# Performance work log

Hardware: AMD Instinct MI355X
Metric: run time of the kernel (lower is better)

The kernel has to match this reference:

```python
import jax, jax.numpy as jnp
import numpy as np

B, T, C, H = 16, 2048, 192, 64

def setup_inputs() -> dict:
    key = jax.random.key(0)
    k1, k2, k3, k4 = jax.random.split(key, 4)
    x = jax.random.normal(k1, (B, T, C), dtype=jnp.float32)
    Wq = jax.random.normal(k2, (C, H), dtype=jnp.float32) * (C ** -0.5)
    Wk = jax.random.normal(k3, (C, H), dtype=jnp.float32) * (C ** -0.5)
    Wv = jax.random.normal(k4, (C, H), dtype=jnp.float32) * (C ** -0.5)
    return {"x": x, "Wq": Wq, "Wk": Wk, "Wv": Wv}

def reference(x, Wq, Wk, Wv):
    # One head of causal self-attention (dropout in eval mode / identity).
    q = x @ Wq                       # [B, T, H]
    k = x @ Wk                       # [B, T, H]
    v = x @ Wv                       # [B, T, H]
    scale = q.shape[-1] ** -0.5
    wei = jnp.einsum('bth,bsh->bts', q, k) * scale   # [B, T, T]
    t = wei.shape[-1]
    causal = jnp.tril(jnp.ones((t, t), dtype=bool))  # tril mask
    wei = jnp.where(causal, wei, -jnp.inf)
    wei = jax.nn.softmax(wei, axis=-1)
    out = jnp.einsum('bts,bsh->bth', wei, v)         # [B, T, H]
    return out
```

## Files before the change

### kernel.cpp

```cpp
#include <hip/hip_runtime.h>

#define B 16
#define T 2048
#define C 192
#define H 64

typedef __bf16 bf16x8 __attribute__((ext_vector_type(8)));
typedef __bf16 bf16x4 __attribute__((ext_vector_type(4)));
typedef float  f32x4  __attribute__((ext_vector_type(4)));

#define MFMA(a, b, c) __builtin_amdgcn_mfma_f32_16x16x32_bf16(a, b, c, 0, 0, 0)

#define SM_BIAS 24.0f

__global__ __launch_bounds__(512) void wtrans_kernel(
    const float* __restrict__ Wq, const float* __restrict__ Wk,
    const float* __restrict__ Wv, __bf16* __restrict__ Wf)
{
    const int idx  = blockIdx.x * 512 + threadIdx.x;
    const int ntg  = idx / 384;
    const int rem  = idx - ntg * 384;
    const int kc   = rem >> 6;
    const int lane = rem & 63;
    const float* Wm = (ntg < 4) ? Wq : (ntg < 8) ? Wk : Wv;
    const int nl = ((ntg & 3) << 4) + (lane & 15);
    const int k0 = kc * 32 + (lane >> 4) * 8;
    bf16x8 d;
    #pragma unroll
    for (int j = 0; j < 8; j++) d[j] = (__bf16)Wm[(k0 + j) * H + nl];
    *(bf16x8*)(Wf + (size_t)idx * 8) = d;
}

__global__ __launch_bounds__(512, 4) void qkv_mfma_kernel(
    const float* __restrict__ x,
    const __bf16* __restrict__ Wf,
    __bf16* __restrict__ qb, __bf16* __restrict__ kb, __bf16* __restrict__ vt)
{
    __shared__ __bf16 tile[64][72];

    const int tid  = threadIdx.x;
    const int w    = tid >> 6;
    const int wg   = w >> 2;
    const int wr   = w & 3;
    const int lane = tid & 63;
    const int lid  = tid & 15;
    const int quad = lane >> 4;
    const int m0   = blockIdx.x * 64 + wr * 16;

    const float* xrow = x + (size_t)(m0 + lid) * C + quad * 8;
    bf16x8 af[6];
    #pragma unroll
    for (int kc = 0; kc < 6; kc++) {
        const float4 a0 = *(const float4*)(xrow + kc * 32);
        const float4 a1 = *(const float4*)(xrow + kc * 32 + 4);
        af[kc][0] = (__bf16)a0.x; af[kc][1] = (__bf16)a0.y;
        af[kc][2] = (__bf16)a0.z; af[kc][3] = (__bf16)a0.w;
        af[kc][4] = (__bf16)a1.x; af[kc][5] = (__bf16)a1.y;
        af[kc][6] = (__bf16)a1.z; af[kc][7] = (__bf16)a1.w;
    }

    f32x4 acc[6] = {};
    #pragma unroll
    for (int kc = 0; kc < 6; kc++)
        #pragma unroll
        for (int nt = 0; nt < 6; nt++) {
            const int ntg = wg * 6 + nt;
            const bf16x8 bfr = *(const bf16x8*)(
                Wf + (((size_t)(ntg * 6 + kc)) * 64 + lane) * 8);
            acc[nt] = MFMA(af[kc], bfr, acc[nt]);
        }

    #pragma unroll
    for (int nt = 0; nt < 6; nt++) {
        const int ntg = wg * 6 + nt;
        const int n = ntg * 16 + lid;
        if (ntg < 8) {
            __bf16* dst = (ntg < 4) ? qb : kb;
            const int col = n & 63;
            const float scale = (ntg < 4) ? 0.1803368801111204f : 1.0f;
            #pragma unroll
            for (int r = 0; r < 4; r++) {
                const int row = m0 + quad * 4 + r;
                dst[(size_t)row * H + col] = (__bf16)(acc[nt][r] * scale);
            }
        } else {
            const int col = n - 128;
            #pragma unroll
            for (int r = 0; r < 4; r++)
                tile[wr * 16 + quad * 4 + r][col] = (__bf16)(acc[nt][r]);
        }
    }
    __syncthreads();

    const int bb = blockIdx.x >> 5;
    const int t0 = (blockIdx.x & 31) << 6;
    {
        const int h   = tid >> 3;
        const int tl0 = (tid & 7) * 8;
        bf16x8 d;
        #pragma unroll
        for (int j = 0; j < 8; j++) d[j] = tile[tl0 + j][h];
        *(bf16x8*)(vt + ((size_t)(bb * H + h)) * T + t0 + tl0) = d;
    }
}

__global__ __launch_bounds__(512, 4) void attn_kernel(
    const __bf16* __restrict__ qb,
    const __bf16* __restrict__ kb,
    const __bf16* __restrict__ vt,
    float* __restrict__ out)
{
    __shared__ __bf16 Kb[2][2][64][72];
    __shared__ __bf16 Vb[2][2][64][68];

    const int tid  = threadIdx.x;
    const int wv   = tid >> 6;
    const int grp  = wv >> 2;
    const int w    = wv & 3;
    const int lid  = tid & 15;
    const int quad = (tid & 63) >> 4;

    const int half = blockIdx.x >> 8;
    const int rem  = blockIdx.x & 255;
    const int b    = rem & 15;
    const int pr   = rem >> 4;
    const int qt   = half ? pr : (31 - pr);
    const int nch  = qt + 1;
    const int nsteps = (nch + 1) >> 1;
    const size_t bbase = (size_t)b * T;

    const int qX = (qt << 6) + w * 16;

    const __bf16* qr = qb + (bbase + qX + lid) * H + quad * 8;
    const bf16x8 qf0 = *(const bf16x8*)(qr);
    const bf16x8 qf1 = *(const bf16x8*)(qr + 32);

    const __bf16* kgb = kb + bbase * H;
    const __bf16* vgb = vt + (size_t)b * H * T;

    const int ra = tid >> 3, ca = (tid & 7) * 8;

    auto keyof = [&](int i) {
        if (i > nch - 1) i = nch - 1;
        return i << 6;
    };

    bf16x8 kr[2], vr2[2];
    auto prefetch = [&](int s) {
        #pragma unroll
        for (int g = 0; g < 2; g++) {
            const int key0 = keyof(2 * s + g);
            kr[g]  = *(const bf16x8*)(kgb + (size_t)(key0 + ra) * H + ca);
            vr2[g] = *(const bf16x8*)(vgb + (size_t)ra * T + key0 + ca);
        }
    };

    f32x4 O[4] = {};
    float ls = 0.f;

    auto doChunk = [&](int key0, int cur) {
        const __bf16 (*Kc)[72] = Kb[cur][grp];
        const __bf16 (*Vc)[68] = Vb[cur][grp];
        bf16x8 kf[8];
        #pragma unroll
        for (int j = 0; j < 4; j++) {
            kf[2*j]   = *(const bf16x8*)&Kc[j * 16 + lid][quad * 8];
            kf[2*j+1] = *(const bf16x8*)&Kc[j * 16 + lid][32 + quad * 8];
        }
        bf16x8 bv0[4], bv1[4];
        #pragma unroll
        for (int ht = 0; ht < 4; ht++) {
            const __bf16* vr_ = &Vc[ht * 16 + lid][quad * 4];
            ((bf16x4*)&bv0[ht])[0] = *(const bf16x4*)(vr_);
            ((bf16x4*)&bv0[ht])[1] = *(const bf16x4*)(vr_ + 16);
            ((bf16x4*)&bv1[ht])[0] = *(const bf16x4*)(vr_ + 32);
            ((bf16x4*)&bv1[ht])[1] = *(const bf16x4*)(vr_ + 48);
        }
        bf16x8 af0, af1;
        const bool boundary = (key0 + 63 > qX);
        #pragma unroll
        for (int j = 0; j < 4; j++) {
            f32x4 sS = {-SM_BIAS, -SM_BIAS, -SM_BIAS, -SM_BIAS};
            sS = MFMA(kf[2*j], qf0, sS);
            sS = MFMA(kf[2*j+1], qf1, sS);
            if (boundary) {
                #pragma unroll
                for (int r = 0; r < 4; r++)
                    if (key0 + j * 16 + quad * 4 + r > qX + lid) sS[r] = -1e30f;
            }
            #pragma unroll
            for (int r = 0; r < 4; r++) {
                const float p = __builtin_amdgcn_exp2f(sS[r]);
                ls += p;
                if      (j == 0) af0[r]     = (__bf16)p;
                else if (j == 1) af0[4 + r] = (__bf16)p;
                else if (j == 2) af1[r]     = (__bf16)p;
                else             af1[4 + r] = (__bf16)p;
            }
        }
        #pragma unroll
        for (int ht = 0; ht < 4; ht++) {
            O[ht] = MFMA(af0, bv0[ht], O[ht]);
            O[ht] = MFMA(af1, bv1[ht], O[ht]);
        }
    };

    prefetch(0);
    int cur = 0;
    for (int s = 0; s < nsteps; s++) {
        *(bf16x8*)&Kb[cur][0][ra][ca] = kr[0];
        *(bf16x8*)&Kb[cur][1][ra][ca] = kr[1];
        *(bf16x8*)&Vb[cur][0][ra][ca] = vr2[0];
        *(bf16x8*)&Vb[cur][1][ra][ca] = vr2[1];
        __syncthreads();
        if (s + 1 < nsteps) prefetch(s + 1);

        const int i = 2 * s + grp;
        if (i < nch) doChunk(i << 6, cur);
        cur ^= 1;
    }

    __syncthreads();
    float* sO = (float*)&Kb[0][0][0][0];
    float* sL = (float*)&Vb[0][0][0][0];

    float l = ls;
    l += __shfl_xor(l, 16, 64);
    l += __shfl_xor(l, 32, 64);

    if (grp == 1) {
        #pragma unroll
        for (int ht = 0; ht < 4; ht++)
            #pragma unroll
            for (int r = 0; r < 4; r++)
                sO[(w * 16 + quad * 4 + r) * 64 + ht * 16 + lid] = O[ht][r];
        if ((tid & 63) < 16) sL[w * 16 + lid] = l;
    }
    __syncthreads();
    if (grp == 0) {
        l += sL[w * 16 + lid];
        #pragma unroll
        for (int ht = 0; ht < 4; ht++)
            #pragma unroll
            for (int r = 0; r < 4; r++) {
                const float Lr = __shfl(l, quad * 4 + r, 16);
                const float v = O[ht][r]
                    + sO[(w * 16 + quad * 4 + r) * 64 + ht * 16 + lid];
                out[(bbase + qX + quad * 4 + r) * H + ht * 16 + lid] = v / Lr;
            }
    }
}

extern "C" void kernel_launch(void* const* d_in, const int* in_sizes, int n_in,
                              void* d_out, int out_size, void* d_ws, size_t ws_size,
                              hipStream_t stream)
{
    const float* x  = (const float*)d_in[0];
    const float* Wq = (const float*)d_in[1];
    const float* Wk = (const float*)d_in[2];
    const float* Wv = (const float*)d_in[3];

    const size_t BTH = (size_t)B * T * H;
    __bf16* qbuf = (__bf16*)d_ws;
    __bf16* kbuf = qbuf + BTH;
    __bf16* vtb  = kbuf + BTH;
    __bf16* Wfb  = vtb + BTH;
    float* outp = (float*)d_out;

    wtrans_kernel<<<9, 512, 0, stream>>>(Wq, Wk, Wv, Wfb);
    qkv_mfma_kernel<<<B * T / 64, 512, 0, stream>>>(x, Wfb, qbuf, kbuf, vtb);
    attn_kernel<<<B * T / 128 * 2, 512, 0, stream>>>(qbuf, kbuf, vtb, outp);
}
```

Before: 106.2 us.

## Repartition attention waves into 32-query by 32-key tiles with two-level reduction

Each wave in the attention kernel previously handled 16 queries against all 64 keys of a chunk. It now handles 32 queries against one 32-key half of the chunk, so every K and V fragment read from LDS feeds two query subtiles. This halves per-wave LDS reads for K and V while keeping the same MFMA count. In exchange each wave holds twice the output accumulators, and the epilogue becomes a two-stage reduction across key halves and wave groups with an extra barrier and padded shared-memory staging.

```diff
diff --git a/kernel.cpp b/kernel.cpp
--- a/kernel.cpp
+++ b/kernel.cpp
@@ -95,12 +95,12 @@
     const int bb = blockIdx.x >> 5;
     const int t0 = (blockIdx.x & 31) << 6;
     {
-        const int h   = tid >> 3;
+        const int hh  = tid >> 3;
         const int tl0 = (tid & 7) * 8;
         bf16x8 d;
         #pragma unroll
-        for (int j = 0; j < 8; j++) d[j] = tile[tl0 + j][h];
-        *(bf16x8*)(vt + ((size_t)(bb * H + h)) * T + t0 + tl0) = d;
+        for (int j = 0; j < 8; j++) d[j] = tile[tl0 + j][hh];
+        *(bf16x8*)(vt + ((size_t)(bb * H + hh)) * T + t0 + tl0) = d;
     }
 }
 
@@ -116,7 +116,10 @@
     const int tid  = threadIdx.x;
     const int wv   = tid >> 6;
     const int grp  = wv >> 2;
-    const int w    = wv & 3;
+    const int wvl  = wv & 3;
+    const int u    = wvl >> 1;
+    const int h    = wvl & 1;
+    const int h32  = h << 5;
     const int lid  = tid & 15;
     const int quad = (tid & 63) >> 4;
 
@@ -129,11 +132,16 @@
     const int nsteps = (nch + 1) >> 1;
     const size_t bbase = (size_t)b * T;
 
-    const int qX = (qt << 6) + w * 16;
-
-    const __bf16* qr = qb + (bbase + qX + lid) * H + quad * 8;
-    const bf16x8 qf0 = *(const bf16x8*)(qr);
-    const bf16x8 qf1 = *(const bf16x8*)(qr + 32);
+    const int qT = qt << 6;
+    const int qU = qT + u * 32;
+
+    bf16x8 qfs[2][2];
+    #pragma unroll
+    for (int qs = 0; qs < 2; qs++) {
+        const __bf16* qr = qb + (bbase + qU + qs * 16 + lid) * H + quad * 8;
+        qfs[qs][0] = *(const bf16x8*)(qr);
+        qfs[qs][1] = *(const bf16x8*)(qr + 32);
+    }
 
     const __bf16* kgb = kb + bbase * H;
     const __bf16* vgb = vt + (size_t)b * H * T;
@@ -155,53 +163,53 @@
         }
     };
 
-    f32x4 O[4] = {};
-    float ls = 0.f;
+    f32x4 O[2][4] = {};
+    float ls[2] = {0.f, 0.f};
 
     auto doChunk = [&](int key0, int cur) {
         const __bf16 (*Kc)[72] = Kb[cur][grp];
         const __bf16 (*Vc)[68] = Vb[cur][grp];
-        bf16x8 kf[8];
-        #pragma unroll
-        for (int j = 0; j < 4; j++) {
-            kf[2*j]   = *(const bf16x8*)&Kc[j * 16 + lid][quad * 8];
-            kf[2*j+1] = *(const bf16x8*)&Kc[j * 16 + lid][32 + quad * 8];
-        }
-        bf16x8 bv0[4], bv1[4];
+        bf16x8 kf[2][2];
+        #pragma unroll
+        for (int j = 0; j < 2; j++) {
+            const __bf16* kp = &Kc[h32 + j * 16 + lid][0];
+            kf[j][0] = *(const bf16x8*)(kp + quad * 8);
+            kf[j][1] = *(const bf16x8*)(kp + 32 + quad * 8);
+        }
+        bf16x8 bv[4];
         #pragma unroll
         for (int ht = 0; ht < 4; ht++) {
-            const __bf16* vr_ = &Vc[ht * 16 + lid][quad * 4];
-            ((bf16x4*)&bv0[ht])[0] = *(const bf16x4*)(vr_);
-            ((bf16x4*)&bv0[ht])[1] = *(const bf16x4*)(vr_ + 16);
-            ((bf16x4*)&bv1[ht])[0] = *(const bf16x4*)(vr_ + 32);
-            ((bf16x4*)&bv1[ht])[1] = *(const bf16x4*)(vr_ + 48);
-        }
-        bf16x8 af0, af1;
-        const bool boundary = (key0 + 63 > qX);
-        #pragma unroll
-        for (int j = 0; j < 4; j++) {
-            f32x4 sS = {-SM_BIAS, -SM_BIAS, -SM_BIAS, -SM_BIAS};
-            sS = MFMA(kf[2*j], qf0, sS);
-            sS = MFMA(kf[2*j+1], qf1, sS);
-            if (boundary) {
-                #pragma unroll
-                for (int r = 0; r < 4; r++)
-                    if (key0 + j * 16 + quad * 4 + r > qX + lid) sS[r] = -1e30f;
+            const __bf16* vp = &Vc[ht * 16 + lid][h32 + quad * 4];
+            ((bf16x4*)&bv[ht])[0] = *(const bf16x4*)(vp);
+            ((bf16x4*)&bv[ht])[1] = *(const bf16x4*)(vp + 16);
+        }
+        const bool boundary = (key0 + h32 + 31 > qU);
+        bf16x8 af[2];
+        #pragma unroll
+        for (int qs = 0; qs < 2; qs++) {
+            #pragma unroll
+            for (int j = 0; j < 2; j++) {
+                f32x4 sS = {-SM_BIAS, -SM_BIAS, -SM_BIAS, -SM_BIAS};
+                sS = MFMA(kf[j][0], qfs[qs][0], sS);
+                sS = MFMA(kf[j][1], qfs[qs][1], sS);
+                if (boundary) {
+                    #pragma unroll
+                    for (int r = 0; r < 4; r++)
+                        if (key0 + h32 + j * 16 + quad * 4 + r >
+                            qU + qs * 16 + lid) sS[r] = -1e30f;
+                }
+                #pragma unroll
+                for (int r = 0; r < 4; r++) {
+                    const float p = __builtin_amdgcn_exp2f(sS[r]);
+                    ls[qs] += p;
+                    af[qs][j * 4 + r] = (__bf16)p;
+                }
             }
-            #pragma unroll
-            for (int r = 0; r < 4; r++) {
-                const float p = __builtin_amdgcn_exp2f(sS[r]);
-                ls += p;
-                if      (j == 0) af0[r]     = (__bf16)p;
-                else if (j == 1) af0[4 + r] = (__bf16)p;
-                else if (j == 2) af1[r]     = (__bf16)p;
-                else             af1[4 + r] = (__bf16)p;
-            }
         }
         #pragma unroll
         for (int ht = 0; ht < 4; ht++) {
-            O[ht] = MFMA(af0, bv0[ht], O[ht]);
-            O[ht] = MFMA(af1, bv1[ht], O[ht]);
+            O[0][ht] = MFMA(af[0], bv[ht], O[0][ht]);
+            O[1][ht] = MFMA(af[1], bv[ht], O[1][ht]);
         }
     };
 
@@ -221,33 +229,75 @@
     }
 
     __syncthreads();
-    float* sO = (float*)&Kb[0][0][0][0];
-    float* sL = (float*)&Vb[0][0][0][0];
-
-    float l = ls;
-    l += __shfl_xor(l, 16, 64);
-    l += __shfl_xor(l, 32, 64);
-
-    if (grp == 1) {
-        #pragma unroll
-        for (int ht = 0; ht < 4; ht++)
-            #pragma unroll
-            for (int r = 0; r < 4; r++)
-                sO[(w * 16 + quad * 4 + r) * 64 + ht * 16 + lid] = O[ht][r];
-        if ((tid & 63) < 16) sL[w * 16 + lid] = l;
+    float* sOp = (float*)&Kb[0][0][0][0];
+    float* sLp = (float*)&Vb[0][0][0][0];
+
+    auto sO = [&](int g_, int u_, int row, int col) -> float& {
+        return sOp[(((g_ * 2 + u_) * 32) + row) * 65 + col];
+    };
+
+    float l0 = ls[0]; l0 += __shfl_xor(l0, 16, 64); l0 += __shfl_xor(l0, 32, 64);
+    float l1 = ls[1]; l1 += __shfl_xor(l1, 16, 64); l1 += __shfl_xor(l1, 32, 64);
+
+    if (h == 1) {
+        #pragma unroll
+        for (int qs = 0; qs < 2; qs++)
+            #pragma unroll
+            for (int ht = 0; ht < 4; ht++)
+                #pragma unroll
+                for (int r = 0; r < 4; r++)
+                    sO(grp, u, qs * 16 + quad * 4 + r, ht * 16 + lid) =
+                        O[qs][ht][r];
+        if ((tid & 63) < 16) {
+            sLp[((grp * 2 + u) * 2 + 0) * 16 + lid] = l0;
+            sLp[((grp * 2 + u) * 2 + 1) * 16 + lid] = l1;
+        }
     }
     __syncthreads();
-    if (grp == 0) {
-        l += sL[w * 16 + lid];
-        #pragma unroll
-        for (int ht = 0; ht < 4; ht++)
-            #pragma unroll
-            for (int r = 0; r < 4; r++) {
-                const float Lr = __shfl(l, quad * 4 + r, 16);
-                const float v = O[ht][r]
-                    + sO[(w * 16 + quad * 4 + r) * 64 + ht * 16 + lid];
-                out[(bbase + qX + quad * 4 + r) * H + ht * 16 + lid] = v / Lr;
+    if (h == 0) {
+        #pragma unroll
+        for (int qs = 0; qs < 2; qs++)
+            #pragma unroll
+            for (int ht = 0; ht < 4; ht++)
+                #pragma unroll
+                for (int r = 0; r < 4; r++)
+                    O[qs][ht][r] +=
+                        sO(grp, u, qs * 16 + quad * 4 + r, ht * 16 + lid);
+        l0 += sLp[((grp * 2 + u) * 2 + 0) * 16 + lid];
+        l1 += sLp[((grp * 2 + u) * 2 + 1) * 16 + lid];
+        if (grp == 1) {
+            #pragma unroll
+            for (int qs = 0; qs < 2; qs++)
+                #pragma unroll
+                for (int ht = 0; ht < 4; ht++)
+                    #pragma unroll
+                    for (int r = 0; r < 4; r++)
+                        sO(1, u, qs * 16 + quad * 4 + r, ht * 16 + lid) =
+                            O[qs][ht][r];
+            if ((tid & 63) < 16) {
+                sLp[128 + (u * 2 + 0) * 16 + lid] = l0;
+                sLp[128 + (u * 2 + 1) * 16 + lid] = l1;
             }
+        }
+    }
+    __syncthreads();
+    if (grp == 0 && h == 0) {
+        l0 += sLp[128 + (u * 2 + 0) * 16 + lid];
+        l1 += sLp[128 + (u * 2 + 1) * 16 + lid];
+        #pragma unroll
+        for (int qs = 0; qs < 2; qs++) {
+            const float lq0 = (qs == 0) ? l0 : l1;
+            #pragma unroll
+            for (int ht = 0; ht < 4; ht++)
+                #pragma unroll
+                for (int r = 0; r < 4; r++) {
+                    const float Lr = __shfl(lq0, quad * 4 + r, 16);
+                    const float v = O[qs][ht][r] +
+                        sO(1, u, qs * 16 + quad * 4 + r, ht * 16 + lid);
+                    out[(bbase + qU + qs * 16 + quad * 4 + r) * H +
+                        ht * 16 + lid] = v / Lr;
+                }
+        }
     }
 }
 
```

Measured after the change: 114.4 us. +7.7%, slower.
